# Optimization experiments

Measured on AMD Instinct MI355X. Metric: run time of the kernel, lower is better.

The kernel has to match this reference:

```python
import jax, jax.numpy as jnp
import numpy as np

B, S, D, H, DF, L, V, MAXLEN = 8, 1024, 768, 12, 3072, 6, 32000, 2048
HD = D // H
EPS = 1e-5

def _pe(max_length, d_model):
    position = jnp.arange(max_length, dtype=jnp.float32)[:, None]
    i = jnp.arange(d_model, dtype=jnp.float32)[None, :]
    angles = position * (1.0 / jnp.power(10000.0, 2.0 * jnp.floor(i / 2.0) / d_model))
    pe = jnp.zeros((max_length, d_model), dtype=jnp.float32)
    pe = pe.at[:, 0::2].set(jnp.sin(angles[:, 0::2]))
    pe = pe.at[:, 1::2].set(jnp.cos(angles[:, 1::2]))
    return pe

def _layernorm(x, g, b):
    mu = jnp.mean(x, axis=-1, keepdims=True)
    var = jnp.mean((x - mu) ** 2, axis=-1, keepdims=True)
    return (x - mu) * jax.lax.rsqrt(var + EPS) * g + b

def setup_inputs() -> dict:
    key = jax.random.key(0)
    ks = jax.random.split(key, 16)
    s = 0.02
    emb = jax.random.normal(ks[0], (V, D), jnp.float32) * s
    emb = emb.at[0].set(0.0)  # padding_idx=0
    inp = {
        'input_ids': jax.random.randint(ks[1], (B, S), 0, V),
        'emb': emb,
        'pe': _pe(MAXLEN, D),
        'Wq': jax.random.normal(ks[2], (L, D, D), jnp.float32) * s,
        'bq': jnp.zeros((L, D), jnp.float32),
        'Wk': jax.random.normal(ks[3], (L, D, D), jnp.float32) * s,
        'bk': jnp.zeros((L, D), jnp.float32),
        'Wv': jax.random.normal(ks[4], (L, D, D), jnp.float32) * s,
        'bv': jnp.zeros((L, D), jnp.float32),
        'W1': jax.random.normal(ks[5], (L, DF, D), jnp.float32) * s,
        'b1': jnp.zeros((L, DF), jnp.float32),
        'W2': jax.random.normal(ks[6], (L, D, DF), jnp.float32) * s,
        'b2': jnp.zeros((L, D), jnp.float32),
        'ln1_g': jnp.ones((L, D), jnp.float32),
        'ln1_b': jnp.zeros((L, D), jnp.float32),
        'ln2_g': jnp.ones((L, D), jnp.float32),
        'ln2_b': jnp.zeros((L, D), jnp.float32),
    }
    return inp

def _mha(x, Wq, bq, Wk, bk, Wv, bv):
    b, s, _ = x.shape
    q = (x @ Wq.T + bq).reshape(b, H, s, HD)  # faithful to torch .view (no transpose)
    k = (x @ Wk.T + bk).reshape(b, H, s, HD)
    v = (x @ Wv.T + bv).reshape(b, H, s, HD)
    scores = jnp.einsum('bhqd,bhkd->bhqk', q, k) / (HD ** 0.5)
    att = jax.nn.softmax(scores, axis=-1)
    o = jnp.einsum('bhqk,bhkd->bhqd', att, v)
    return o.transpose(0, 2, 1, 3).reshape(b, s, D)

def reference(input_ids, emb, pe, Wq, bq, Wk, bk, Wv, bv, W1, b1, W2, b2, ln1_g, ln1_b, ln2_g, ln2_b):
    x = emb[input_ids] + pe[:input_ids.shape[1], :]
    # dropout is identity in eval mode
    for l in range(L):
        h1 = _mha(x, Wq[l], bq[l], Wk[l], bk[l], Wv[l], bv[l])
        y1 = _layernorm(x + h1, ln1_g[l], ln1_b[l])
        h2 = jax.nn.relu(y1 @ W1[l].T + b1[l]) @ W2[l].T + b2[l]
        x = _layernorm(y1 + h2, ln2_g[l], ln2_b[l])
    return x
```

## Files before the change

kernel.cpp:

```cpp
#include <hip/hip_runtime.h>


typedef _Float16 f16;
typedef _Float16 half8 __attribute__((ext_vector_type(8)));
typedef float f32x4 __attribute__((ext_vector_type(4)));
typedef float f32x16 __attribute__((ext_vector_type(16)));

constexpr int Bn = 8, Sn = 1024, Dn = 768, Hn = 12, HDn = 64, DFn = 3072, Ln = 6;
constexpr int BS = Bn * Sn;

__device__ __forceinline__ void glds16(const f16* g, f16* l) {
  __builtin_amdgcn_global_load_lds(
      (const __attribute__((address_space(1))) unsigned int*)g,
      (__attribute__((address_space(3))) unsigned int*)l, 16, 0, 0);
}

__device__ __forceinline__ float ex2(float x) {
#if __has_builtin(__builtin_amdgcn_exp2f)
  return __builtin_amdgcn_exp2f(x);
#else
  return exp2f(x);
#endif
}

__global__ __launch_bounds__(256) void pack_qkv(
    const float* __restrict__ Wq, const float* __restrict__ Wk, const float* __restrict__ Wv,
    const float* __restrict__ bq, const float* __restrict__ bk, const float* __restrict__ bv,
    f16* __restrict__ Wo, float* __restrict__ bo) {
  const long per = (long)Dn * Dn;
  long i = (long)blockIdx.x * 256 + threadIdx.x;
  const long totalW = (long)Ln * 3 * per;
  if (i < totalW) {
    int l = (int)(i / (3 * per));
    long rem = i - (long)l * 3 * per;
    int which = (int)(rem / per);
    long e = rem - (long)which * per;
    const float* s = (which == 0) ? Wq : ((which == 1) ? Wk : Wv);
    Wo[i] = (f16)(s[(long)l * per + e]);
  }
  if (i < (long)Ln * 3 * Dn) {
    int l = (int)(i / (3 * Dn));
    int rem = (int)(i % (3 * Dn));
    int which = rem / Dn, c = rem % Dn;
    const float* s = (which == 0) ? bq : ((which == 1) ? bk : bv);
    bo[i] = s[l * Dn + c];
  }
}

__global__ __launch_bounds__(256) void f32_to_f16_k(
    const float* __restrict__ src, f16* __restrict__ dst, long n) {
  long i = ((long)blockIdx.x * 256 + threadIdx.x) * 4;
  if (i < n) {
    float4 v = *(const float4*)&src[i];
    dst[i + 0] = (f16)v.x;
    dst[i + 1] = (f16)v.y;
    dst[i + 2] = (f16)v.z;
    dst[i + 3] = (f16)v.w;
  }
}

__global__ __launch_bounds__(256) void embed_k(
    const int* __restrict__ ids, const float* __restrict__ emb, const float* __restrict__ pe,
    float* __restrict__ Xf, f16* __restrict__ Xh) {
  const int row = blockIdx.x;
  const int s = row & (Sn - 1);
  const int id = ids[row];
  const size_t eb = (size_t)id * Dn, pb = (size_t)s * Dn, ob = (size_t)row * Dn;
  for (int c = threadIdx.x; c < Dn; c += 256) {
    float v = emb[eb + c] + pe[pb + c];
    Xf[ob + c] = v;
    Xh[ob + c] = (f16)v;
  }
}

template <int MODE>
__global__ __launch_bounds__(256) void gemm_bt(
    const f16* __restrict__ A, const f16* __restrict__ Bw, const float* __restrict__ bias,
    float* __restrict__ outF, f16* __restrict__ o0, f16* __restrict__ o1, f16* __restrict__ o2,
    int M, int N, int K) {
  const int m0 = blockIdx.x * 128;
  const int n0 = blockIdx.y * 128;
  const int tid = threadIdx.x;
  const int lane = tid & 63, wave = tid >> 6;
  const int wm = wave & 1, wn = wave >> 1;
  const int l15 = lane & 15, l4 = lane >> 4;

  __shared__ __align__(16) f16 As[128 * 32];
  __shared__ __align__(16) f16 Bs[128 * 32];

  const f32x4 z4 = {0.f, 0.f, 0.f, 0.f};
  f32x4 acc[4][4];
#pragma unroll
  for (int i = 0; i < 4; i++)
#pragma unroll
    for (int j = 0; j < 4; j++) acc[i][j] = z4;

  const int sRow = wave * 32 + (lane >> 2);
  const int sCol = (lane & 3) * 8;
  const f16* gA = A + (size_t)(m0 + sRow) * K + sCol;
  const f16* gB = Bw + (size_t)(n0 + sRow) * K + sCol;
  f16* lA0 = &As[(wave * 32) * 32];
  f16* lA1 = &As[(wave * 32 + 16) * 32];
  f16* lB0 = &Bs[(wave * 32) * 32];
  f16* lB1 = &Bs[(wave * 32 + 16) * 32];
  const size_t rowStep = (size_t)16 * K;

  const int kr = 8 * l4;
  for (int k0 = 0; k0 < K; k0 += 32) {
    glds16(gA + k0, lA0);
    glds16(gA + k0 + rowStep, lA1);
    glds16(gB + k0, lB0);
    glds16(gB + k0 + rowStep, lB1);
    __syncthreads();
    half8 af[4], bfr[4];
#pragma unroll
    for (int i = 0; i < 4; i++) af[i] = *(const half8*)&As[(wm * 64 + i * 16 + l15) * 32 + kr];
#pragma unroll
    for (int j = 0; j < 4; j++) bfr[j] = *(const half8*)&Bs[(wn * 64 + j * 16 + l15) * 32 + kr];
#pragma unroll
    for (int i = 0; i < 4; i++)
#pragma unroll
      for (int j = 0; j < 4; j++)
        acc[i][j] = __builtin_amdgcn_mfma_f32_16x16x32_f16(af[i], bfr[j], acc[i][j], 0, 0, 0);
    __syncthreads();
  }

  const int colb = n0 + wn * 64;
  const int rowb = m0 + wm * 64;
#pragma unroll
  for (int j = 0; j < 4; j++) {
    const int col = colb + j * 16 + l15;
    const float bb = bias[col];
#pragma unroll
    for (int i = 0; i < 4; i++) {
      const int rb = rowb + i * 16 + l4 * 4;
#pragma unroll
      for (int r = 0; r < 4; r++) {
        float v = acc[i][j][r] + bb;
        const int row = rb + r;
        if (MODE == 1) v = fmaxf(v, 0.f);
        if (MODE == 2) {
          outF[(size_t)row * N + col] = v;
        } else if (MODE == 3) {
          const int sel = col / 768;
          const int cl = col - sel * 768;
          f16* op = (sel == 0) ? o0 : ((sel == 1) ? o1 : o2);
          op[(size_t)row * 768 + cl] = (f16)v;
        } else {
          o0[(size_t)row * N + col] = (f16)v;
        }
      }
    }
  }
}

__global__ __launch_bounds__(256, 3) void attn_k(
    const f16* __restrict__ Qg, const f16* __restrict__ Kg, const f16* __restrict__ Vg,
    float* __restrict__ O) {
  const int bh = blockIdx.x;
  const int q0 = blockIdx.y * 128;
  const int b = bh / Hn, h = bh - b * Hn;
  const size_t base = (size_t)b * (Sn * Dn) + (size_t)h * (Sn * HDn);
  const f16* Qh = Qg + base;
  const f16* Kh = Kg + base;
  const f16* Vh = Vg + base;

  const int tid = threadIdx.x, lane = tid & 63, wave = tid >> 6;
  const int l31 = lane & 31;
  const int hi = lane >> 5;

  __shared__ __align__(16) f16 Ks[64 * 72];
  __shared__ __align__(16) f16 Vt[64 * 72];

  const int qrow = q0 + wave * 32 + l31;
  half8 qf[4];
#pragma unroll
  for (int m = 0; m < 4; m++)
    qf[m] = *(const half8*)&Qh[(size_t)qrow * HDn + 16 * m + 8 * hi];

  f32x16 Oacc0, Oacc1;
#pragma unroll
  for (int i = 0; i < 16; i++) { Oacc0[i] = 0.f; Oacc1[i] = 0.f; }
  float mrow = -1e30f, lrow = 0.f;
  const float csc = 0.18033688011112042f;

  for (int kt = 0; kt < Sn / 64; ++kt) {
#pragma unroll
    for (int cc = 0; cc < 2; cc++) {
      const int c = tid + cc * 256;
      const int row = c >> 3, col = (c & 7) * 8;
      *(int4*)&Ks[row * 72 + col] = *(const int4*)&Kh[(size_t)(kt * 64 + row) * HDn + col];
    }
#pragma unroll
    for (int ee = 0; ee < 2; ee++) {
      const int e = tid + ee * 256;
      const int hd = e & 63, kpo = e >> 6;
      f16 tmp[8];
#pragma unroll
      for (int j = 0; j < 8; j++)
        tmp[j] = Vh[(size_t)(kt * 64 + kpo * 8 + j) * HDn + hd];
      *(int4*)&Vt[hd * 72 + kpo * 8] = *(const int4*)tmp;
    }
    __syncthreads();

    f32x16 s0, s1;
#pragma unroll
    for (int i = 0; i < 16; i++) { s0[i] = 0.f; s1[i] = 0.f; }
#pragma unroll
    for (int m = 0; m < 4; m++) {
      half8 k0 = *(const half8*)&Ks[l31 * 72 + 16 * m + 8 * hi];
      half8 k1 = *(const half8*)&Ks[(32 + l31) * 72 + 16 * m + 8 * hi];
      s0 = __builtin_amdgcn_mfma_f32_32x32x16_f16(k0, qf[m], s0, 0, 0, 0);
      s1 = __builtin_amdgcn_mfma_f32_32x32x16_f16(k1, qf[m], s1, 0, 0, 0);
    }

    float t8[8];
#pragma unroll
    for (int i = 0; i < 8; i++)
      t8[i] = fmaxf(fmaxf(s0[i], s0[i + 8]), fmaxf(s1[i], s1[i + 8]));
#pragma unroll
    for (int i = 0; i < 4; i++) t8[i] = fmaxf(t8[i], t8[i + 4]);
    float mx = fmaxf(fmaxf(t8[0], t8[1]), fmaxf(t8[2], t8[3]));
    mx = fmaxf(mx, __shfl_xor(mx, 32));
    const float M = fmaxf(mrow, mx * csc);
    const float alpha = ex2(mrow - M);

#pragma unroll
    for (int i = 0; i < 16; i++) {
      s0[i] = ex2(fmaf(s0[i], csc, -M));
      s1[i] = ex2(fmaf(s1[i], csc, -M));
    }
    float r0 = 0.f, r1 = 0.f, r2 = 0.f, r3 = 0.f;
#pragma unroll
    for (int i = 0; i < 16; i += 4) {
      r0 += s0[i]; r1 += s0[i + 1]; r2 += s0[i + 2]; r3 += s0[i + 3];
      r0 += s1[i]; r1 += s1[i + 1]; r2 += s1[i + 2]; r3 += s1[i + 3];
    }
    float rsum = (r0 + r1) + (r2 + r3);
    rsum += __shfl_xor(rsum, 32);
    lrow = lrow * alpha + rsum;
    mrow = M;
#pragma unroll
    for (int i = 0; i < 16; i++) { Oacc0[i] *= alpha; Oacc1[i] *= alpha; }

    unsigned pA[2][4], pB[2][4];
#pragma unroll
    for (int t = 0; t < 4; t++) {
      pA[0][t] = __builtin_bit_cast(unsigned, __builtin_amdgcn_cvt_pkrtz(s0[4 * t + 0], s0[4 * t + 1]));
      pB[0][t] = __builtin_bit_cast(unsigned, __builtin_amdgcn_cvt_pkrtz(s0[4 * t + 2], s0[4 * t + 3]));
      pA[1][t] = __builtin_bit_cast(unsigned, __builtin_amdgcn_cvt_pkrtz(s1[4 * t + 0], s1[4 * t + 1]));
      pB[1][t] = __builtin_bit_cast(unsigned, __builtin_amdgcn_cvt_pkrtz(s1[4 * t + 2], s1[4 * t + 3]));
    }

#pragma unroll
    for (int c = 0; c < 4; c++) {
      const int g = c >> 1, tt = 2 * (c & 1);
      const unsigned ownA = hi ? pA[g][tt + 1] : pA[g][tt];
      const unsigned ownB = hi ? pB[g][tt + 1] : pB[g][tt];
      const unsigned sndA = hi ? pA[g][tt] : pA[g][tt + 1];
      const unsigned sndB = hi ? pB[g][tt] : pB[g][tt + 1];
      const unsigned rA = (unsigned)__shfl_xor((int)sndA, 32);
      const unsigned rB = (unsigned)__shfl_xor((int)sndB, 32);
      int4 w;
      w.x = (int)(hi ? rA : ownA);
      w.y = (int)(hi ? rB : ownB);
      w.z = (int)(hi ? ownA : rA);
      w.w = (int)(hi ? ownB : rB);
      const half8 pf = __builtin_bit_cast(half8, w);
      const half8 v0 = *(const half8*)&Vt[l31 * 72 + 16 * c + 8 * hi];
      const half8 v1 = *(const half8*)&Vt[(32 + l31) * 72 + 16 * c + 8 * hi];
      Oacc0 = __builtin_amdgcn_mfma_f32_32x32x16_f16(v0, pf, Oacc0, 0, 0, 0);
      Oacc1 = __builtin_amdgcn_mfma_f32_32x32x16_f16(v1, pf, Oacc1, 0, 0, 0);
    }
    __syncthreads();
  }

  const float inv = 1.f / lrow;
  float* Orow = O + ((size_t)b * Sn + qrow) * Dn + h * HDn;
#pragma unroll
  for (int t = 0; t < 4; t++) {
    float4 o0, o1;
    o0.x = Oacc0[4 * t + 0] * inv; o0.y = Oacc0[4 * t + 1] * inv;
    o0.z = Oacc0[4 * t + 2] * inv; o0.w = Oacc0[4 * t + 3] * inv;
    o1.x = Oacc1[4 * t + 0] * inv; o1.y = Oacc1[4 * t + 1] * inv;
    o1.z = Oacc1[4 * t + 2] * inv; o1.w = Oacc1[4 * t + 3] * inv;
    *(float4*)&Orow[8 * t + 4 * hi] = o0;
    *(float4*)&Orow[32 + 8 * t + 4 * hi] = o1;
  }
}

__global__ __launch_bounds__(256) void add_ln(
    const float* __restrict__ Xi, const float* __restrict__ Hr,
    const float* __restrict__ g, const float* __restrict__ bt,
    float* __restrict__ Yf, f16* __restrict__ Yh) {
  const int row = blockIdx.x;
  const int tid = threadIdx.x;
  const size_t base = (size_t)row * Dn;
  float v0 = Xi[base + tid] + Hr[base + tid];
  float v1 = Xi[base + tid + 256] + Hr[base + tid + 256];
  float v2 = Xi[base + tid + 512] + Hr[base + tid + 512];

  __shared__ float red[8];
  float s = v0 + v1 + v2;
  for (int off = 32; off; off >>= 1) s += __shfl_down(s, off);
  const int wv = tid >> 6, ln = tid & 63;
  if (ln == 0) red[wv] = s;
  __syncthreads();
  if (tid == 0) red[4] = (red[0] + red[1] + red[2] + red[3]) * (1.f / Dn);
  __syncthreads();
  const float mu = red[4];
  const float d0 = v0 - mu, d1 = v1 - mu, d2 = v2 - mu;
  float vs = d0 * d0 + d1 * d1 + d2 * d2;
  for (int off = 32; off; off >>= 1) vs += __shfl_down(vs, off);
  if (ln == 0) red[wv] = vs;
  __syncthreads();
  if (tid == 0) red[5] = rsqrtf((red[0] + red[1] + red[2] + red[3]) * (1.f / Dn) + 1e-5f);
  __syncthreads();
  const float rs = red[5];
  float y0 = d0 * rs * g[tid] + bt[tid];
  float y1 = d1 * rs * g[tid + 256] + bt[tid + 256];
  float y2 = d2 * rs * g[tid + 512] + bt[tid + 512];
  Yf[base + tid] = y0;        Yh[base + tid] = (f16)y0;
  Yf[base + tid + 256] = y1;  Yh[base + tid + 256] = (f16)y1;
  Yf[base + tid + 512] = y2;  Yh[base + tid + 512] = (f16)y2;
}

extern "C" void kernel_launch(void* const* d_in, const int* in_sizes, int n_in,
                              void* d_out, int out_size, void* d_ws, size_t ws_size,
                              hipStream_t stream) {
  const int* ids  = (const int*)d_in[0];
  const float* emb = (const float*)d_in[1];
  const float* pe  = (const float*)d_in[2];
  const float* Wq  = (const float*)d_in[3];
  const float* bq  = (const float*)d_in[4];
  const float* Wk  = (const float*)d_in[5];
  const float* bk  = (const float*)d_in[6];
  const float* Wv  = (const float*)d_in[7];
  const float* bv  = (const float*)d_in[8];
  const float* W1  = (const float*)d_in[9];
  const float* b1  = (const float*)d_in[10];
  const float* W2  = (const float*)d_in[11];
  const float* b2  = (const float*)d_in[12];
  const float* g1  = (const float*)d_in[13];
  const float* be1 = (const float*)d_in[14];
  const float* g2  = (const float*)d_in[15];
  const float* be2 = (const float*)d_in[16];
  float* out = (float*)d_out;

  char* w = (char*)d_ws;
  auto alloc = [&](size_t bytes) {
    char* p = w;
    w += (bytes + 255) & ~(size_t)255;
    return p;
  };
  f16* Wqkv  = (f16*)alloc((size_t)Ln * 3 * Dn * Dn * 2);
  float* bqkv = (float*)alloc((size_t)Ln * 3 * Dn * 4);
  f16* W1h   = (f16*)alloc((size_t)Ln * DFn * Dn * 2);
  f16* W2h   = (f16*)alloc((size_t)Ln * Dn * DFn * 2);
  float* Xf  = (float*)alloc((size_t)BS * Dn * 4);
  f16* Xh    = (f16*)alloc((size_t)BS * Dn * 2);
  f16* Qh    = (f16*)alloc((size_t)BS * Dn * 2);
  f16* Kh    = (f16*)alloc((size_t)BS * Dn * 2);
  f16* Vh    = (f16*)alloc((size_t)BS * Dn * 2);
  float* Of  = (float*)alloc((size_t)BS * Dn * 4);
  float* Y1f = (float*)alloc((size_t)BS * Dn * 4);
  f16* Y1h   = (f16*)alloc((size_t)BS * Dn * 2);
  f16* F1h   = (f16*)alloc((size_t)BS * DFn * 2);
  float* H2f = (float*)alloc((size_t)BS * Dn * 4);

  {
    const int gw = (Ln * 3 * Dn * Dn + 255) / 256;
    pack_qkv<<<gw, 256, 0, stream>>>(Wq, Wk, Wv, bq, bk, bv, Wqkv, bqkv);
    const long n1 = (long)Ln * DFn * Dn;
    const int gc = (int)(n1 / 4 / 256);
    f32_to_f16_k<<<gc, 256, 0, stream>>>(W1, W1h, n1);
    f32_to_f16_k<<<gc, 256, 0, stream>>>(W2, W2h, n1);
  }

  embed_k<<<BS, 256, 0, stream>>>(ids, emb, pe, Xf, Xh);

  for (int l = 0; l < Ln; ++l) {
    gemm_bt<3><<<dim3(BS / 128, (3 * Dn) / 128), 256, 0, stream>>>(
        Xh, Wqkv + (size_t)l * 3 * Dn * Dn, bqkv + l * 3 * Dn,
        nullptr, Qh, Kh, Vh, BS, 3 * Dn, Dn);

    attn_k<<<dim3(Bn * Hn, Sn / 128), 256, 0, stream>>>(Qh, Kh, Vh, Of);

    add_ln<<<BS, 256, 0, stream>>>(Xf, Of, g1 + l * Dn, be1 + l * Dn, Y1f, Y1h);

    gemm_bt<1><<<dim3(BS / 128, DFn / 128), 256, 0, stream>>>(
        Y1h, W1h + (size_t)l * DFn * Dn, b1 + l * DFn,
        nullptr, F1h, nullptr, nullptr, BS, DFn, Dn);

    gemm_bt<2><<<dim3(BS / 128, Dn / 128), 256, 0, stream>>>(
        F1h, W2h + (size_t)l * Dn * DFn, b2 + l * Dn,
        H2f, nullptr, nullptr, nullptr, BS, Dn, DFn);

    float* dstF = (l == Ln - 1) ? out : Xf;
    add_ln<<<BS, 256, 0, stream>>>(Y1f, H2f, g2 + l * Dn, be2 + l * Dn, dstF, Xh);
  }
}
```

Measured before the change: 2.069 ms.

## Split-K the FFN down-projection GEMM and fuse partial reduction into layernorm

The W2 GEMM (N=768, K=3072) now runs as a two-way split-K launch via a new MODE 4, writing fp32 partials into a scratch region aliased over the dead Q/K/V/O buffers. The new add_ln_sk2 kernel sums the two partials, adds the bias and the residual, then applies layernorm. The aim is more blocks and better CU balance on the small-N GEMM, at the cost of extra partial write and read traffic. The weight conversion kernels also switch to vectorized half4 stores.

```diff
diff --git a/kernel.cpp b/kernel.cpp
--- a/kernel.cpp
+++ b/kernel.cpp
@@ -2,6 +2,7 @@
 
 
 typedef _Float16 f16;
+typedef _Float16 half4 __attribute__((ext_vector_type(4)));
 typedef _Float16 half8 __attribute__((ext_vector_type(8)));
 typedef float f32x4 __attribute__((ext_vector_type(4)));
 typedef float f32x16 __attribute__((ext_vector_type(16)));
@@ -28,22 +29,25 @@
     const float* __restrict__ bq, const float* __restrict__ bk, const float* __restrict__ bv,
     f16* __restrict__ Wo, float* __restrict__ bo) {
   const long per = (long)Dn * Dn;
-  long i = (long)blockIdx.x * 256 + threadIdx.x;
-  const long totalW = (long)Ln * 3 * per;
-  if (i < totalW) {
-    int l = (int)(i / (3 * per));
+  const long t = (long)blockIdx.x * 256 + threadIdx.x;
+  const long totalW4 = (long)Ln * 3 * per / 4;
+  if (t < totalW4) {
+    const long i = t * 4;
+    const int l = (int)(i / (3 * per));
     long rem = i - (long)l * 3 * per;
-    int which = (int)(rem / per);
-    long e = rem - (long)which * per;
+    const int which = (int)(rem / per);
+    const long e = rem - (long)which * per;
     const float* s = (which == 0) ? Wq : ((which == 1) ? Wk : Wv);
-    Wo[i] = (f16)(s[(long)l * per + e]);
-  }
-  if (i < (long)Ln * 3 * Dn) {
-    int l = (int)(i / (3 * Dn));
-    int rem = (int)(i % (3 * Dn));
+    const float4 v = *(const float4*)&s[(long)l * per + e];
+    half4 h = {(f16)v.x, (f16)v.y, (f16)v.z, (f16)v.w};
+    *(half4*)&Wo[i] = h;
+  }
+  if (t < (long)Ln * 3 * Dn) {
+    int l = (int)(t / (3 * Dn));
+    int rem = (int)(t % (3 * Dn));
     int which = rem / Dn, c = rem % Dn;
     const float* s = (which == 0) ? bq : ((which == 1) ? bk : bv);
-    bo[i] = s[l * Dn + c];
+    bo[t] = s[l * Dn + c];
   }
 }
 
@@ -52,10 +56,8 @@
   long i = ((long)blockIdx.x * 256 + threadIdx.x) * 4;
   if (i < n) {
     float4 v = *(const float4*)&src[i];
-    dst[i + 0] = (f16)v.x;
-    dst[i + 1] = (f16)v.y;
-    dst[i + 2] = (f16)v.z;
-    dst[i + 3] = (f16)v.w;
+    half4 h = {(f16)v.x, (f16)v.y, (f16)v.z, (f16)v.w};
+    *(half4*)&dst[i] = h;
   }
 }
 
@@ -77,7 +79,7 @@
 __global__ __launch_bounds__(256) void gemm_bt(
     const f16* __restrict__ A, const f16* __restrict__ Bw, const float* __restrict__ bias,
     float* __restrict__ outF, f16* __restrict__ o0, f16* __restrict__ o1, f16* __restrict__ o2,
-    int M, int N, int K) {
+    int M, int N, int K, int lda) {
   const int m0 = blockIdx.x * 128;
   const int n0 = blockIdx.y * 128;
   const int tid = threadIdx.x;
@@ -97,13 +99,14 @@
 
   const int sRow = wave * 32 + (lane >> 2);
   const int sCol = (lane & 3) * 8;
-  const f16* gA = A + (size_t)(m0 + sRow) * K + sCol;
-  const f16* gB = Bw + (size_t)(n0 + sRow) * K + sCol;
+  const int kz = (MODE == 4) ? ((int)blockIdx.z * K) : 0;
+  const f16* gA = A + (size_t)(m0 + sRow) * lda + kz + sCol;
+  const f16* gB = Bw + (size_t)(n0 + sRow) * lda + kz + sCol;
   f16* lA0 = &As[(wave * 32) * 32];
   f16* lA1 = &As[(wave * 32 + 16) * 32];
   f16* lB0 = &Bs[(wave * 32) * 32];
   f16* lB1 = &Bs[(wave * 32 + 16) * 32];
-  const size_t rowStep = (size_t)16 * K;
+  const size_t rowStep = (size_t)16 * lda;
 
   const int kr = 8 * l4;
   for (int k0 = 0; k0 < K; k0 += 32) {
@@ -130,7 +133,7 @@
 #pragma unroll
   for (int j = 0; j < 4; j++) {
     const int col = colb + j * 16 + l15;
-    const float bb = bias[col];
+    const float bb = (MODE == 4) ? 0.f : bias[col];
 #pragma unroll
     for (int i = 0; i < 4; i++) {
       const int rb = rowb + i * 16 + l4 * 4;
@@ -138,14 +141,16 @@
       for (int r = 0; r < 4; r++) {
         float v = acc[i][j][r] + bb;
         const int row = rb + r;
-        if (MODE == 1) v = fmaxf(v, 0.f);
-        if (MODE == 2) {
-          outF[(size_t)row * N + col] = v;
+        if (MODE == 1) {
+          v = fmaxf(v, 0.f);
+          o0[(size_t)row * N + col] = (f16)v;
         } else if (MODE == 3) {
           const int sel = col / 768;
           const int cl = col - sel * 768;
           f16* op = (sel == 0) ? o0 : ((sel == 1) ? o1 : o2);
           op[(size_t)row * 768 + cl] = (f16)v;
+        } else if (MODE == 4) {
+          outF[((size_t)blockIdx.z * M + row) * N + col] = v;
         } else {
           o0[(size_t)row * N + col] = (f16)v;
         }
@@ -299,6 +304,43 @@
   float v0 = Xi[base + tid] + Hr[base + tid];
   float v1 = Xi[base + tid + 256] + Hr[base + tid + 256];
   float v2 = Xi[base + tid + 512] + Hr[base + tid + 512];
+
+  __shared__ float red[8];
+  float s = v0 + v1 + v2;
+  for (int off = 32; off; off >>= 1) s += __shfl_down(s, off);
+  const int wv = tid >> 6, ln = tid & 63;
+  if (ln == 0) red[wv] = s;
+  __syncthreads();
+  if (tid == 0) red[4] = (red[0] + red[1] + red[2] + red[3]) * (1.f / Dn);
+  __syncthreads();
+  const float mu = red[4];
+  const float d0 = v0 - mu, d1 = v1 - mu, d2 = v2 - mu;
+  float vs = d0 * d0 + d1 * d1 + d2 * d2;
+  for (int off = 32; off; off >>= 1) vs += __shfl_down(vs, off);
+  if (ln == 0) red[wv] = vs;
+  __syncthreads();
+  if (tid == 0) red[5] = rsqrtf((red[0] + red[1] + red[2] + red[3]) * (1.f / Dn) + 1e-5f);
+  __syncthreads();
+  const float rs = red[5];
+  float y0 = d0 * rs * g[tid] + bt[tid];
+  float y1 = d1 * rs * g[tid + 256] + bt[tid + 256];
+  float y2 = d2 * rs * g[tid + 512] + bt[tid + 512];
+  Yf[base + tid] = y0;        Yh[base + tid] = (f16)y0;
+  Yf[base + tid + 256] = y1;  Yh[base + tid + 256] = (f16)y1;
+  Yf[base + tid + 512] = y2;  Yh[base + tid + 512] = (f16)y2;
+}
+
+__global__ __launch_bounds__(256) void add_ln_sk2(
+    const float* __restrict__ Xi, const float* __restrict__ P,
+    const float* __restrict__ b2, const float* __restrict__ g, const float* __restrict__ bt,
+    float* __restrict__ Yf, f16* __restrict__ Yh) {
+  const int row = blockIdx.x;
+  const int tid = threadIdx.x;
+  const size_t base = (size_t)row * Dn;
+  const size_t cs = (size_t)BS * Dn;
+  float v0 = Xi[base + tid]       + P[base + tid]       + P[cs + base + tid]       + b2[tid];
+  float v1 = Xi[base + tid + 256] + P[base + tid + 256] + P[cs + base + tid + 256] + b2[tid + 256];
+  float v2 = Xi[base + tid + 512] + P[base + tid + 512] + P[cs + base + tid + 512] + b2[tid + 512];
 
   __shared__ float red[8];
   float s = v0 + v1 + v2;
@@ -366,10 +408,12 @@
   float* Y1f = (float*)alloc((size_t)BS * Dn * 4);
   f16* Y1h   = (f16*)alloc((size_t)BS * Dn * 2);
   f16* F1h   = (f16*)alloc((size_t)BS * DFn * 2);
-  float* H2f = (float*)alloc((size_t)BS * Dn * 4);
+
+  float* Pf = (float*)Qh;
 
   {
-    const int gw = (Ln * 3 * Dn * Dn + 255) / 256;
+    const long totalW4 = (long)Ln * 3 * Dn * Dn / 4;
+    const int gw = (int)((totalW4 + 255) / 256);
     pack_qkv<<<gw, 256, 0, stream>>>(Wq, Wk, Wv, bq, bk, bv, Wqkv, bqkv);
     const long n1 = (long)Ln * DFn * Dn;
     const int gc = (int)(n1 / 4 / 256);
@@ -382,7 +426,7 @@
   for (int l = 0; l < Ln; ++l) {
     gemm_bt<3><<<dim3(BS / 128, (3 * Dn) / 128), 256, 0, stream>>>(
         Xh, Wqkv + (size_t)l * 3 * Dn * Dn, bqkv + l * 3 * Dn,
-        nullptr, Qh, Kh, Vh, BS, 3 * Dn, Dn);
+        nullptr, Qh, Kh, Vh, BS, 3 * Dn, Dn, Dn);
 
     attn_k<<<dim3(Bn * Hn, Sn / 128), 256, 0, stream>>>(Qh, Kh, Vh, Of);
 
@@ -390,13 +434,14 @@
 
     gemm_bt<1><<<dim3(BS / 128, DFn / 128), 256, 0, stream>>>(
         Y1h, W1h + (size_t)l * DFn * Dn, b1 + l * DFn,
-        nullptr, F1h, nullptr, nullptr, BS, DFn, Dn);
-
-    gemm_bt<2><<<dim3(BS / 128, Dn / 128), 256, 0, stream>>>(
-        F1h, W2h + (size_t)l * Dn * DFn, b2 + l * Dn,
-        H2f, nullptr, nullptr, nullptr, BS, Dn, DFn);
+        nullptr, F1h, nullptr, nullptr, BS, DFn, Dn, Dn);
+
+    gemm_bt<4><<<dim3(BS / 128, Dn / 128, 2), 256, 0, stream>>>(
+        F1h, W2h + (size_t)l * Dn * DFn, nullptr,
+        Pf, nullptr, nullptr, nullptr, BS, Dn, DFn / 2, DFn);
 
     float* dstF = (l == Ln - 1) ? out : Xf;
-    add_ln<<<BS, 256, 0, stream>>>(Y1f, H2f, g2 + l * Dn, be2 + l * Dn, dstF, Xh);
-  }
-}
+    add_ln_sk2<<<BS, 256, 0, stream>>>(Y1f, Pf, b2 + l * Dn,
+                                       g2 + l * Dn, be2 + l * Dn, dstF, Xh);
+  }
+}
```

Result: faster. 1.927 ms (-6.9%).
